# Kernel optimization log

Measured on AMD Instinct MI355X. Metric: run time of the kernel, lower is better.

Reference implementation:

```python
import jax, jax.numpy as jnp
import numpy as np

B, T, D = 4, 2048, 256
KQ, V, H = 16, 16, 8
SCALE = float(np.sqrt(KQ))


def _lin(key, din, dout):
    k1, k2 = jax.random.split(key)
    lim = 1.0 / np.sqrt(din)
    w = jax.random.uniform(k1, (din, dout), minval=-lim, maxval=lim, dtype=jnp.float32)
    b = jax.random.uniform(k2, (dout,), minval=-lim, maxval=lim, dtype=jnp.float32)
    return w, b


def setup_inputs() -> dict:
    key = jax.random.key(0)
    ks = jax.random.split(key, 14)
    x = jax.random.normal(ks[0], (B, 3, T), dtype=jnp.float32)
    h = jax.random.normal(ks[1], (B, D, T), dtype=jnp.float32)
    q_w1, q_b1 = _lin(ks[2], D, KQ * H)
    q_w2, q_b2 = _lin(ks[3], KQ * H, KQ * H)
    k_w1, k_b1 = _lin(ks[4], D, KQ * H)
    k_w2, k_b2 = _lin(ks[5], KQ * H, KQ * H)
    v_w1, v_b1 = _lin(ks[6], D, V * H)
    v_w2, v_b2 = _lin(ks[7], V * H, V * H)
    xm_w1, xm_b1 = _lin(ks[8], V * H, V * H)
    xm_w2, xm_b2 = _lin(ks[9], V * H, H)
    ho_w, ho_b = _lin(ks[10], V * H, D)
    # GVP: Wh [v_in, dim_h], Wu [dim_h, v_out]; torch init = randn
    gvp_Wh = jax.random.normal(ks[11], (H, H), dtype=jnp.float32)
    gvp_Wu = jax.random.normal(ks[12], (H, 1), dtype=jnp.float32)
    return dict(x=x, h=h,
                q_w1=q_w1, q_b1=q_b1, q_w2=q_w2, q_b2=q_b2,
                k_w1=k_w1, k_b1=k_b1, k_w2=k_w2, k_b2=k_b2,
                v_w1=v_w1, v_b1=v_b1, v_w2=v_w2, v_b2=v_b2,
                xm_w1=xm_w1, xm_b1=xm_b1, xm_w2=xm_w2, xm_b2=xm_b2,
                ho_w=ho_w, ho_b=ho_b, gvp_Wh=gvp_Wh, gvp_Wu=gvp_Wu)


def _mlp(x, w1, b1, w2, b2):
    return jax.nn.silu(x @ w1 + b1) @ w2 + b2


def _rotate_half(t):
    # interleaved pairs (x1,x2) -> (-x2, x1), lucidrains rotary convention
    t2 = t.reshape(t.shape[:-1] + (t.shape[-1] // 2, 2))
    a, b = t2[..., 0], t2[..., 1]
    return jnp.stack((-b, a), axis=-1).reshape(t.shape)


def _rope(t):
    # t: [B, H, T, KQ]
    seq = t.shape[-2]
    inv = 1.0 / (10000.0 ** (jnp.arange(0, KQ, 2, dtype=jnp.float32) / KQ))
    f = jnp.arange(seq, dtype=jnp.float32)[:, None] * inv[None, :]   # [T, KQ/2]
    f = jnp.repeat(f, 2, axis=-1)                                    # [T, KQ]
    return t * jnp.cos(f) + _rotate_half(t) * jnp.sin(f)


def _forward(x, h,
             q_w1, q_b1, q_w2, q_b2,
             k_w1, k_b1, k_w2, k_b2,
             v_w1, v_b1, v_w2, v_b2,
             xm_w1, xm_b1, xm_w2, xm_b2,
             ho_w, ho_b, gvp_Wh, gvp_Wu):
    b, _, t = x.shape
    h_m = jnp.transpose(h, (0, 2, 1)).reshape(b * t, D)     # merge_time_dim
    q = _mlp(h_m, q_w1, q_b1, q_w2, q_b2)                   # [B*T, KQ*H]
    k = _mlp(h_m, k_w1, k_b1, k_w2, k_b2)
    v = _mlp(h_m, v_w1, v_b1, v_w2, v_b2)                   # [B*T, V*H]
    v_x = _mlp(v, xm_w1, xm_b1, xm_w2, xm_b2)               # [B*T, H]

    q = q.reshape(b, t, H, KQ).transpose(0, 2, 1, 3)        # [B,H,T,KQ]
    k = k.reshape(b, t, H, KQ).transpose(0, 2, 1, 3)
    v4 = v.reshape(b, t, H, V).transpose(0, 2, 1, 3)        # [B,H,T,V]
    v_x = v_x.reshape(b, t, H).transpose(0, 2, 1)           # [B,H,T]

    q = _rope(q)
    k = _rope(k)

    attn = jax.nn.softmax(
        jnp.einsum('bhtd,bhsd->bhts', q, k) / SCALE, axis=-1)  # [B,H,T,T]

    h_upd = jnp.einsum('bhts,bhsd->bhtd', attn, v4)         # [B,H,T,V]
    h_upd = h_upd.transpose(0, 2, 1, 3).reshape(b, t, H * V)
    h_upd = (h_upd @ ho_w + ho_b).transpose(0, 2, 1)        # [B,D,T]
    h_out = h + h_upd

    attn_w = attn * v_x[:, :, None, :]                      # weight key axis s
    gamma = attn_w.sum(axis=-1)                             # [B,H,T]
    weighted_x = jnp.einsum('bhij,bdj->bhdi', attn_w, x)    # [B,H,3,T]
    x_head = gamma[:, :, None, :] * x[:, None, :, :] - weighted_x  # [B,H,3,T]
    x_upd = x_head.transpose(0, 3, 1, 2).reshape(b * t, H, 3)      # [B*T,H,3]

    # GVP vector branch (scalar branch does not affect returned vectors)
    Vh = jnp.einsum('bvc,vh->bhc', x_upd, gvp_Wh)           # [B*T,H,3]
    Vu = jnp.einsum('bhc,hu->buc', Vh, gvp_Wu)              # [B*T,1,3]
    gate = jnp.linalg.norm(Vu, axis=-1, keepdims=True)      # [B*T,1,1]
    delta = jax.nn.sigmoid(gate) * Vu                       # [B*T,1,3]
    delta = delta[:, 0, :].reshape(b, t, 3).transpose(0, 2, 1)  # separate_time_dim -> [B,3,T]
    x_out = x + delta
    return x_out, h_out


def reference(x, h,
              q_w1, q_b1, q_w2, q_b2,
              k_w1, k_b1, k_w2, k_b2,
              v_w1, v_b1, v_w2, v_b2,
              xm_w1, xm_b1, xm_w2, xm_b2,
              ho_w, ho_b, gvp_Wh, gvp_Wu):
    return _forward(x, h,
                    q_w1, q_b1, q_w2, q_b2,
                    k_w1, k_b1, k_w2, k_b2,
                    v_w1, v_b1, v_w2, v_b2,
                    xm_w1, xm_b1, xm_w2, xm_b2,
                    ho_w, ho_b, gvp_Wh, gvp_Wu)
```

## Files before the change

### kernel.cpp

```cpp
#include <hip/hip_runtime.h>
#include <hip/hip_bf16.h>
#include <math.h>

typedef __attribute__((ext_vector_type(8))) short s16x8;
typedef __attribute__((ext_vector_type(4))) float f32x4;

__device__ __forceinline__ float silu(float a) {
    return a / (1.f + __expf(-a));
}
__device__ __forceinline__ unsigned short f2b(float f) {
    __hip_bfloat16 h = __float2bfloat16(f);
    return *reinterpret_cast<unsigned short*>(&h);
}

__global__ __launch_bounds__(256) void wprep(
    const float* __restrict__ qw1, const float* __restrict__ kw1,
    const float* __restrict__ vw1, const float* __restrict__ qw2,
    const float* __restrict__ kw2, const float* __restrict__ vw2,
    const float* __restrict__ xmw1, const float* __restrict__ xmw2,
    const float* __restrict__ how,
    unsigned short* __restrict__ w1T, unsigned short* __restrict__ w2T,
    unsigned short* __restrict__ xm1T, unsigned short* __restrict__ xm2T,
    unsigned short* __restrict__ howT)
{
    int idx = blockIdx.x * 256 + threadIdx.x;
    if (idx < 98304) {
        int m = idx >> 15, r = idx & 32767;
        int n = r >> 8, k = r & 255;
        const float* src = (m == 0) ? qw1 : (m == 1) ? kw1 : vw1;
        w1T[idx] = f2b(src[k * 128 + n]);
    } else if (idx < 147456) {
        int r0 = idx - 98304;
        int m = r0 >> 14, r = r0 & 16383;
        int n = r >> 7, k = r & 127;
        const float* src = (m == 0) ? qw2 : (m == 1) ? kw2 : vw2;
        w2T[r0] = f2b(src[k * 128 + n]);
    } else if (idx < 163840) {
        int r = idx - 147456;
        int n = r >> 7, k = r & 127;
        xm1T[r] = f2b(xmw1[k * 128 + n]);
    } else if (idx < 165888) {
        int r = idx - 163840;
        int n = r >> 7, k = r & 127;
        xm2T[r] = (n < 8) ? f2b(xmw2[k * 8 + n]) : (unsigned short)0;
    } else if (idx < 198656) {
        int r = idx - 165888;
        int n = r >> 7, k = r & 127;
        howT[r] = f2b(how[k * 256 + n]);
    }
}

__global__ __launch_bounds__(256) void qkv_mfma(
    const float* __restrict__ x, const float* __restrict__ h,
    const float* __restrict__ qb1, const float* __restrict__ qb2,
    const float* __restrict__ kb1, const float* __restrict__ kb2,
    const float* __restrict__ vb1, const float* __restrict__ vb2,
    const float* __restrict__ xmb1, const float* __restrict__ xmb2,
    const unsigned short* __restrict__ w1T, const unsigned short* __restrict__ w2T,
    const unsigned short* __restrict__ xm1T, const unsigned short* __restrict__ xm2T,
    unsigned short* __restrict__ q_bf, unsigned short* __restrict__ k_bf,
    unsigned short* __restrict__ vT_bf)
{
    const int blk = blockIdx.x;
    const int b   = blk >> 7;
    const int t0  = (blk & 127) << 4;
    const int tid = threadIdx.x;
    const int nq   = tid >> 6;
    const int lane = tid & 63;
    const int m_   = lane & 15;
    const int quad = lane >> 4;

    __shared__ __align__(16) unsigned short hA[16][264];
    __shared__ __align__(16) unsigned short hidQ[16][136];
    __shared__ __align__(16) unsigned short hidK[16][136];
    __shared__ __align__(16) unsigned short hidV[16][136];
    __shared__ __align__(16) unsigned short voutA[16][136];
    __shared__ float vxs[16][8];

    #pragma unroll
    for (int g = 0; g < 4; g++) {
        float4 hv = *(const float4*)(h + ((size_t)(b * 256 + tid)) * 2048
                                       + t0 + g * 4);
        hA[g * 4 + 0][tid] = f2b(hv.x);
        hA[g * 4 + 1][tid] = f2b(hv.y);
        hA[g * 4 + 2][tid] = f2b(hv.z);
        hA[g * 4 + 3][tid] = f2b(hv.w);
    }
    __syncthreads();

    const f32x4 zero = {0.f, 0.f, 0.f, 0.f};

    {
        f32x4 aQ[2] = {zero, zero}, aK[2] = {zero, zero}, aV[2] = {zero, zero};
        #pragma unroll
        for (int kc = 0; kc < 8; kc++) {
            s16x8 af = *(const s16x8*)&hA[m_][kc * 32 + quad * 8];
            #pragma unroll
            for (int nt = 0; nt < 2; nt++) {
                size_t woff = (size_t)(nq * 32 + nt * 16 + m_) * 256
                            + kc * 32 + quad * 8;
                aQ[nt] = __builtin_amdgcn_mfma_f32_16x16x32_bf16(
                    af, *(const s16x8*)(w1T + woff), aQ[nt], 0, 0, 0);
                aK[nt] = __builtin_amdgcn_mfma_f32_16x16x32_bf16(
                    af, *(const s16x8*)(w1T + 32768 + woff), aK[nt], 0, 0, 0);
                aV[nt] = __builtin_amdgcn_mfma_f32_16x16x32_bf16(
                    af, *(const s16x8*)(w1T + 65536 + woff), aV[nt], 0, 0, 0);
            }
        }
        #pragma unroll
        for (int nt = 0; nt < 2; nt++) {
            int col = nq * 32 + nt * 16 + m_;
            float bq = qb1[col], bk = kb1[col], bv = vb1[col];
            #pragma unroll
            for (int i = 0; i < 4; i++) {
                hidQ[quad * 4 + i][col] = f2b(silu(aQ[nt][i] + bq));
                hidK[quad * 4 + i][col] = f2b(silu(aK[nt][i] + bk));
                hidV[quad * 4 + i][col] = f2b(silu(aV[nt][i] + bv));
            }
        }
    }
    __syncthreads();

    auto gemm2 = [&](const unsigned short* w2m,
                     unsigned short (*hid)[136], f32x4 acc[2]) {
        #pragma unroll
        for (int kc = 0; kc < 4; kc++) {
            s16x8 af = *(const s16x8*)&hid[m_][kc * 32 + quad * 8];
            #pragma unroll
            for (int nt = 0; nt < 2; nt++) {
                const s16x8 bf = *(const s16x8*)(w2m
                    + (size_t)(nq * 32 + nt * 16 + m_) * 128 + kc * 32 + quad * 8);
                acc[nt] = __builtin_amdgcn_mfma_f32_16x16x32_bf16(
                    af, bf, acc[nt], 0, 0, 0);
            }
        }
    };
    auto rope_store = [&](f32x4 acc[2], const float* b2,
                          unsigned short* dst, float scale) {
        #pragma unroll
        for (int nt = 0; nt < 2; nt++) {
            int col  = nq * 32 + nt * 16 + m_;
            int head = col >> 4, dim = col & 15;
            float inv = exp2f(-(float)(dim >> 1) * 0.125f * 13.28771238f);
            float bia = b2[col];
            #pragma unroll
            for (int i = 0; i < 4; i++) {
                int t = t0 + quad * 4 + i;
                float a  = acc[nt][i] + bia;
                float pr = __shfl_xor(a, 1);
                float f  = (float)t * inv;
                float cs = cosf(f), sn = sinf(f);
                float o  = (dim & 1) ? (a * cs + pr * sn) : (a * cs - pr * sn);
                dst[((size_t)(b * 8 + head) * 2048 + t) * 16 + dim] =
                    f2b(o * scale);
            }
        }
    };

    {
        f32x4 aQ[2] = {zero, zero}, aK[2] = {zero, zero}, aV[2] = {zero, zero};
        gemm2(w2T,         hidQ, aQ);
        gemm2(w2T + 16384, hidK, aK);
        gemm2(w2T + 32768, hidV, aV);
        rope_store(aQ, qb2, q_bf, 0.25f);
        rope_store(aK, kb2, k_bf, 1.0f);
        #pragma unroll
        for (int nt = 0; nt < 2; nt++) {
            int col = nq * 32 + nt * 16 + m_;
            float bia = vb2[col];
            #pragma unroll
            for (int i = 0; i < 4; i++)
                voutA[quad * 4 + i][col] = f2b(aV[nt][i] + bia);
        }
    }
    __syncthreads();

    {
        int col = tid >> 1, tg = tid & 1;
        s16x8 pk;
        #pragma unroll
        for (int e = 0; e < 8; e++)
            pk[e] = (short)voutA[tg * 8 + e][col];
        *(s16x8*)(vT_bf + ((size_t)(b * 8 + (col >> 4)) * 32 + (col & 15)) * 2048
                        + t0 + tg * 8) = pk;
    }
    {
        f32x4 acc[2] = {zero, zero};
        #pragma unroll
        for (int kc = 0; kc < 4; kc++) {
            s16x8 af = *(const s16x8*)&voutA[m_][kc * 32 + quad * 8];
            #pragma unroll
            for (int nt = 0; nt < 2; nt++) {
                const s16x8 bf = *(const s16x8*)(xm1T
                    + (size_t)(nq * 32 + nt * 16 + m_) * 128 + kc * 32 + quad * 8);
                acc[nt] = __builtin_amdgcn_mfma_f32_16x16x32_bf16(
                    af, bf, acc[nt], 0, 0, 0);
            }
        }
        #pragma unroll
        for (int nt = 0; nt < 2; nt++) {
            int col = nq * 32 + nt * 16 + m_;
            float bia = xmb1[col];
            #pragma unroll
            for (int i = 0; i < 4; i++)
                hidQ[quad * 4 + i][col] = f2b(silu(acc[nt][i] + bia));
        }
    }
    __syncthreads();

    if (nq == 0) {
        f32x4 a2 = zero;
        #pragma unroll
        for (int kc = 0; kc < 4; kc++) {
            s16x8 af = *(const s16x8*)&hidQ[m_][kc * 32 + quad * 8];
            const s16x8 bf = *(const s16x8*)(xm2T
                + (size_t)m_ * 128 + kc * 32 + quad * 8);
            a2 = __builtin_amdgcn_mfma_f32_16x16x32_bf16(af, bf, a2, 0, 0, 0);
        }
        if (m_ < 8) {
            float bia = xmb2[m_];
            #pragma unroll
            for (int i = 0; i < 4; i++)
                vxs[quad * 4 + i][m_] = a2[i] + bia;
        }
    }
    __syncthreads();

    #pragma unroll
    for (int r = 0; r < 2; r++) {
        int i  = tid + r * 256;
        int hh = i >> 6, c = (i >> 4) & 3, tt = i & 15;
        float val = vxs[tt][hh];
        if (c)
            val *= x[((size_t)(b * 3 + (c - 1))) * 2048 + t0 + tt];
        vT_bf[((size_t)(b * 8 + hh) * 32 + 16 + c) * 2048 + t0 + tt] = f2b(val);
    }
    if (tid < 192) {
        int hh = tid / 24, rem = tid % 24;
        int c  = 20 + (rem >> 1), tg = rem & 1;
        s16x8 z = {0,0,0,0,0,0,0,0};
        *(s16x8*)(vT_bf + ((size_t)(b * 8 + hh) * 32 + c) * 2048
                        + t0 + tg * 8) = z;
    }
}

__global__ __launch_bounds__(64) void attn_mfma(
    const unsigned short* __restrict__ q_bf,
    const unsigned short* __restrict__ k_bf,
    const unsigned short* __restrict__ vT_bf,
    float* __restrict__ opart)
{
    const int blk  = blockIdx.x;
    const int sp   = blk >> 10;
    const int bh   = (blk >> 5) & 31;
    const int qs   = (blk & 31) << 6;
    const int lane = threadIdx.x;
    const int m_   = lane & 15;
    const int quad = lane >> 4;

    __shared__ __align__(16) unsigned short Elds[4][2][16 * 72];

    const s16x8 zs = {0, 0, 0, 0, 0, 0, 0, 0};
    const f32x4 zero = {0.f, 0.f, 0.f, 0.f};

    s16x8 qfrag[4];
    #pragma unroll
    for (int qt = 0; qt < 4; qt++) {
        qfrag[qt] = zs;
        if (quad < 2)
            qfrag[qt] = *(const s16x8*)(q_bf +
                ((size_t)(bh * 2048 + qs + qt * 16 + m_) * 16 + quad * 8));
    }

    f32x4 O0[4], O1[4];
    float lsq[4];
    #pragma unroll
    for (int qt = 0; qt < 4; qt++) {
        O0[qt] = zero; O1[qt] = zero; lsq[qt] = 0.f;
    }

    const unsigned short* kb = k_bf + ((size_t)bh * 2048 + sp * 1024) * 16;
    const unsigned short* vb = vT_bf + (size_t)bh * 32 * 2048 + sp * 1024;

    for (int kt = 0; kt < 16; kt++) {
        const int k0 = kt * 64;
        const int buf = kt & 1;

        s16x8 kf[4];
        #pragma unroll
        for (int n = 0; n < 4; n++) {
            kf[n] = zs;
            if (quad < 2)
                kf[n] = *(const s16x8*)(kb +
                      ((size_t)(k0 + n * 16 + m_) * 16 + quad * 8));
        }
        s16x8 vf0[2], vf1[2];
        #pragma unroll
        for (int c = 0; c < 2; c++) {
            vf0[c] = *(const s16x8*)(vb + (size_t)m_ * 2048
                                        + k0 + c * 32 + quad * 8);
            vf1[c] = *(const s16x8*)(vb + (size_t)(16 + m_) * 2048
                                        + k0 + c * 32 + quad * 8);
        }

        #pragma unroll
        for (int qt = 0; qt < 4; qt++) {
            #pragma unroll
            for (int n = 0; n < 4; n++) {
                f32x4 E = __builtin_amdgcn_mfma_f32_16x16x32_bf16(
                    kf[n], qfrag[qt], zero, 0, 0, 0);
                float e0 = __expf(E[0]);
                float e1 = __expf(E[1]);
                float e2 = __expf(E[2]);
                float e3 = __expf(E[3]);
                lsq[qt] += e0 + e1 + e2 + e3;
                uint2 pk;
                pk.x = (unsigned)f2b(e0) | ((unsigned)f2b(e1) << 16);
                pk.y = (unsigned)f2b(e2) | ((unsigned)f2b(e3) << 16);
                *(uint2*)&Elds[qt][buf][m_ * 72 + n * 16 + quad * 4] = pk;
            }
        }
        __builtin_amdgcn_s_waitcnt(0xc07f);

        #pragma unroll
        for (int qt = 0; qt < 4; qt++) {
            #pragma unroll
            for (int c = 0; c < 2; c++) {
                s16x8 af = *(const s16x8*)
                    &Elds[qt][buf][m_ * 72 + c * 32 + quad * 8];
                O0[qt] = __builtin_amdgcn_mfma_f32_16x16x32_bf16(
                    af, vf0[c], O0[qt], 0, 0, 0);
                O1[qt] = __builtin_amdgcn_mfma_f32_16x16x32_bf16(
                    af, vf1[c], O1[qt], 0, 0, 0);
            }
        }
    }

    #pragma unroll
    for (int qt = 0; qt < 4; qt++) {
        float s = lsq[qt];
        s += __shfl_xor(s, 16);
        s += __shfl_xor(s, 32);
        float* opb = opart + ((size_t)(sp * 32 + bh) * 2048 + qs + qt * 16) * 24;
        #pragma unroll
        for (int i = 0; i < 4; i++) {
            int row = quad * 4 + i;
            float* ob = opb + row * 24;
            ob[m_] = O0[qt][i];
            if (m_ < 4) ob[16 + m_] = O1[qt][i];
        }
        if (quad == 0) opb[m_ * 24 + 20] = s;
    }
}

__global__ __launch_bounds__(256) void epi_kernel(
    const float* __restrict__ opart, const unsigned short* __restrict__ howT,
    const float* __restrict__ x, const float* __restrict__ hin,
    const float* __restrict__ hob,
    const float* __restrict__ Wh, const float* __restrict__ Wu,
    float* __restrict__ out)
{
    const int blk = blockIdx.x;
    const int b  = blk >> 7;
    const int t0 = (blk & 127) << 4;
    const int tid = threadIdx.x;
    const int nq   = tid >> 6;
    const int lane = tid & 63;
    const int m_   = lane & 15;
    const int quad = lane >> 4;
    const size_t half = (size_t)32 * 2048 * 24;

    __shared__ __align__(16) unsigned short hvA[16][136];
    __shared__ float linv[8][16];
    __shared__ float gamma[8][16], wx[8][3][16];
    __shared__ float weff[8];

    if (tid < 128) {
        int hh = tid >> 4, tt = tid & 15;
        size_t off = ((size_t)(b * 8 + hh) * 2048 + t0 + tt) * 24 + 20;
        linv[hh][tt] = 1.f / (opart[off] + opart[half + off]);
    } else if (tid < 136) {
        int v = tid - 128;
        float s = 0.f;
        for (int j = 0; j < 8; j++) s += Wh[v * 8 + j] * Wu[j];
        weff[v] = s;
    }
    __syncthreads();

    #pragma unroll
    for (int r = 0; r < 8; r++) {
        int i = tid + r * 256;
        int jj = i >> 4, tt = i & 15;
        size_t off = ((size_t)(b * 8 + (jj >> 4)) * 2048 + t0 + tt) * 24
                   + (jj & 15);
        hvA[tt][jj] =
            f2b((opart[off] + opart[half + off]) * linv[jj >> 4][tt]);
    }
    #pragma unroll
    for (int r = 0; r < 2; r++) {
        int i = tid + r * 256;
        int hh = i >> 6, c = (i >> 4) & 3, tt = i & 15;
        size_t off = ((size_t)(b * 8 + hh) * 2048 + t0 + tt) * 24 + 16 + c;
        float v = (opart[off] + opart[half + off]) * linv[hh][tt];
        if (c == 0) gamma[hh][tt] = v; else wx[hh][c - 1][tt] = v;
    }
    __syncthreads();

    const f32x4 zero = {0.f, 0.f, 0.f, 0.f};
    #pragma unroll
    for (int nt = 0; nt < 4; nt++) {
        int col = nq * 64 + nt * 16 + m_;
        f32x4 acc = zero;
        #pragma unroll
        for (int kc = 0; kc < 4; kc++) {
            s16x8 af = *(const s16x8*)&hvA[m_][kc * 32 + quad * 8];
            const s16x8 bf = *(const s16x8*)(howT
                + (size_t)col * 128 + kc * 32 + quad * 8);
            acc = __builtin_amdgcn_mfma_f32_16x16x32_bf16(af, bf, acc, 0, 0, 0);
        }
        float bia = hob[col];
        size_t base = ((size_t)b * 256 + col) * 2048 + t0 + quad * 4;
        float4 hold = *(const float4*)(hin + base);
        float4 hres;
        hres.x = hold.x + acc[0] + bia;
        hres.y = hold.y + acc[1] + bia;
        hres.z = hold.z + acc[2] + bia;
        hres.w = hold.w + acc[3] + bia;
        *(float4*)(out + 24576 + base) = hres;
    }

    if (tid < 16) {
        int tt = tid;
        int t = t0 + tt;
        float Vu[3], xv[3];
        #pragma unroll
        for (int c = 0; c < 3; c++) {
            xv[c] = x[((size_t)b * 3 + c) * 2048 + t];
            float s = 0.f;
            #pragma unroll
            for (int v = 0; v < 8; v++)
                s += (gamma[v][tt] * xv[c] - wx[v][c][tt]) * weff[v];
            Vu[c] = s;
        }
        float gate = sqrtf(Vu[0]*Vu[0] + Vu[1]*Vu[1] + Vu[2]*Vu[2]);
        float sg = 1.f / (1.f + __expf(-gate));
        #pragma unroll
        for (int c = 0; c < 3; c++)
            out[((size_t)b * 3 + c) * 2048 + t] = xv[c] + sg * Vu[c];
    }
}

extern "C" void kernel_launch(void* const* d_in, const int* in_sizes, int n_in,
                              void* d_out, int out_size, void* d_ws,
                              size_t ws_size, hipStream_t stream)
{
    const float* x    = (const float*)d_in[0];
    const float* h    = (const float*)d_in[1];
    const float* qw1  = (const float*)d_in[2];
    const float* qb1  = (const float*)d_in[3];
    const float* qw2  = (const float*)d_in[4];
    const float* qb2  = (const float*)d_in[5];
    const float* kw1  = (const float*)d_in[6];
    const float* kb1  = (const float*)d_in[7];
    const float* kw2  = (const float*)d_in[8];
    const float* kb2  = (const float*)d_in[9];
    const float* vw1  = (const float*)d_in[10];
    const float* vb1  = (const float*)d_in[11];
    const float* vw2  = (const float*)d_in[12];
    const float* vb2  = (const float*)d_in[13];
    const float* xmw1 = (const float*)d_in[14];
    const float* xmb1 = (const float*)d_in[15];
    const float* xmw2 = (const float*)d_in[16];
    const float* xmb2 = (const float*)d_in[17];
    const float* how  = (const float*)d_in[18];
    const float* hob  = (const float*)d_in[19];
    const float* Wh   = (const float*)d_in[20];
    const float* Wu   = (const float*)d_in[21];
    float* out = (float*)d_out;

    unsigned short* q_bf  = (unsigned short*)d_ws;
    unsigned short* k_bf  = q_bf + (size_t)32 * 2048 * 16;
    unsigned short* vT_bf = k_bf + (size_t)32 * 2048 * 16;
    float* opart = (float*)(vT_bf + (size_t)32 * 32 * 2048);
    unsigned short* w1T  = (unsigned short*)(opart + (size_t)2 * 32 * 2048 * 24);
    unsigned short* w2T  = w1T + 98304;
    unsigned short* xm1T = w2T + 49152;
    unsigned short* xm2T = xm1T + 16384;
    unsigned short* howT = xm2T + 2048;

    wprep<<<776, 256, 0, stream>>>(qw1, kw1, vw1, qw2, kw2, vw2, xmw1, xmw2,
                                   how, w1T, w2T, xm1T, xm2T, howT);
    qkv_mfma<<<512, 256, 0, stream>>>(
        x, h, qb1, qb2, kb1, kb2, vb1, vb2, xmb1, xmb2,
        w1T, w2T, xm1T, xm2T, q_bf, k_bf, vT_bf);
    attn_mfma<<<2048, 64, 0, stream>>>(q_bf, k_bf, vT_bf, opart);
    epi_kernel<<<512, 256, 0, stream>>>(opart, howT, x, h, hob, Wh, Wu, out);
}
```

Baseline: 183.9 us.

## Split QKV projection into per-role blocks and attention keys into four splits

The QKV kernel now launches three times as many blocks, and each block computes only one of Q, K or V. Only V blocks continue into the xm MLP path. Attention splits the key range four ways instead of two, doubling the attention grid, and the epilogue sums four partial buffers. The aim is more parallelism and occupancy on a wide GPU. The cost is that every QKV block reloads the h tile three times and there is extra partial-sum traffic, which needs larger workspace.

```diff
diff --git a/kernel.cpp b/kernel.cpp
--- a/kernel.cpp
+++ b/kernel.cpp
@@ -61,19 +61,19 @@
     unsigned short* __restrict__ q_bf, unsigned short* __restrict__ k_bf,
     unsigned short* __restrict__ vT_bf)
 {
-    const int blk = blockIdx.x;
-    const int b   = blk >> 7;
-    const int t0  = (blk & 127) << 4;
-    const int tid = threadIdx.x;
+    const int blk  = blockIdx.x;
+    const int role = blk >> 9;
+    const int tb   = blk & 511;
+    const int b    = tb >> 7;
+    const int t0   = (tb & 127) << 4;
+    const int tid  = threadIdx.x;
     const int nq   = tid >> 6;
     const int lane = tid & 63;
     const int m_   = lane & 15;
     const int quad = lane >> 4;
 
     __shared__ __align__(16) unsigned short hA[16][264];
-    __shared__ __align__(16) unsigned short hidQ[16][136];
-    __shared__ __align__(16) unsigned short hidK[16][136];
-    __shared__ __align__(16) unsigned short hidV[16][136];
+    __shared__ __align__(16) unsigned short hidA[16][136];
     __shared__ __align__(16) unsigned short voutA[16][136];
     __shared__ float vxs[16][8];
 
@@ -89,54 +89,51 @@
     __syncthreads();
 
     const f32x4 zero = {0.f, 0.f, 0.f, 0.f};
+    const float* b1 = (role == 0) ? qb1 : (role == 1) ? kb1 : vb1;
+    const float* b2 = (role == 0) ? qb2 : (role == 1) ? kb2 : vb2;
+    const unsigned short* w1m = w1T + role * 32768;
+    const unsigned short* w2m = w2T + role * 16384;
 
     {
-        f32x4 aQ[2] = {zero, zero}, aK[2] = {zero, zero}, aV[2] = {zero, zero};
+        f32x4 acc[2] = {zero, zero};
         #pragma unroll
         for (int kc = 0; kc < 8; kc++) {
             s16x8 af = *(const s16x8*)&hA[m_][kc * 32 + quad * 8];
             #pragma unroll
             for (int nt = 0; nt < 2; nt++) {
-                size_t woff = (size_t)(nq * 32 + nt * 16 + m_) * 256
-                            + kc * 32 + quad * 8;
-                aQ[nt] = __builtin_amdgcn_mfma_f32_16x16x32_bf16(
-                    af, *(const s16x8*)(w1T + woff), aQ[nt], 0, 0, 0);
-                aK[nt] = __builtin_amdgcn_mfma_f32_16x16x32_bf16(
-                    af, *(const s16x8*)(w1T + 32768 + woff), aK[nt], 0, 0, 0);
-                aV[nt] = __builtin_amdgcn_mfma_f32_16x16x32_bf16(
-                    af, *(const s16x8*)(w1T + 65536 + woff), aV[nt], 0, 0, 0);
-            }
-        }
-        #pragma unroll
-        for (int nt = 0; nt < 2; nt++) {
-            int col = nq * 32 + nt * 16 + m_;
-            float bq = qb1[col], bk = kb1[col], bv = vb1[col];
-            #pragma unroll
-            for (int i = 0; i < 4; i++) {
-                hidQ[quad * 4 + i][col] = f2b(silu(aQ[nt][i] + bq));
-                hidK[quad * 4 + i][col] = f2b(silu(aK[nt][i] + bk));
-                hidV[quad * 4 + i][col] = f2b(silu(aV[nt][i] + bv));
-            }
-        }
-    }
-    __syncthreads();
-
-    auto gemm2 = [&](const unsigned short* w2m,
-                     unsigned short (*hid)[136], f32x4 acc[2]) {
-        #pragma unroll
-        for (int kc = 0; kc < 4; kc++) {
-            s16x8 af = *(const s16x8*)&hid[m_][kc * 32 + quad * 8];
-            #pragma unroll
-            for (int nt = 0; nt < 2; nt++) {
-                const s16x8 bf = *(const s16x8*)(w2m
-                    + (size_t)(nq * 32 + nt * 16 + m_) * 128 + kc * 32 + quad * 8);
+                const s16x8 bf = *(const s16x8*)(w1m
+                    + (size_t)(nq * 32 + nt * 16 + m_) * 256 + kc * 32 + quad * 8);
                 acc[nt] = __builtin_amdgcn_mfma_f32_16x16x32_bf16(
                     af, bf, acc[nt], 0, 0, 0);
             }
         }
-    };
-    auto rope_store = [&](f32x4 acc[2], const float* b2,
-                          unsigned short* dst, float scale) {
+        #pragma unroll
+        for (int nt = 0; nt < 2; nt++) {
+            int col = nq * 32 + nt * 16 + m_;
+            float bia = b1[col];
+            #pragma unroll
+            for (int i = 0; i < 4; i++)
+                hidA[quad * 4 + i][col] = f2b(silu(acc[nt][i] + bia));
+        }
+    }
+    __syncthreads();
+
+    f32x4 acc[2] = {zero, zero};
+    #pragma unroll
+    for (int kc = 0; kc < 4; kc++) {
+        s16x8 af = *(const s16x8*)&hidA[m_][kc * 32 + quad * 8];
+        #pragma unroll
+        for (int nt = 0; nt < 2; nt++) {
+            const s16x8 bf = *(const s16x8*)(w2m
+                + (size_t)(nq * 32 + nt * 16 + m_) * 128 + kc * 32 + quad * 8);
+            acc[nt] = __builtin_amdgcn_mfma_f32_16x16x32_bf16(
+                af, bf, acc[nt], 0, 0, 0);
+        }
+    }
+
+    if (role < 2) {
+        unsigned short* dst = (role == 0) ? q_bf : k_bf;
+        float scale = (role == 0) ? 0.25f : 1.0f;
         #pragma unroll
         for (int nt = 0; nt < 2; nt++) {
             int col  = nq * 32 + nt * 16 + m_;
@@ -155,23 +152,16 @@
                     f2b(o * scale);
             }
         }
-    };
-
-    {
-        f32x4 aQ[2] = {zero, zero}, aK[2] = {zero, zero}, aV[2] = {zero, zero};
-        gemm2(w2T,         hidQ, aQ);
-        gemm2(w2T + 16384, hidK, aK);
-        gemm2(w2T + 32768, hidV, aV);
-        rope_store(aQ, qb2, q_bf, 0.25f);
-        rope_store(aK, kb2, k_bf, 1.0f);
-        #pragma unroll
-        for (int nt = 0; nt < 2; nt++) {
-            int col = nq * 32 + nt * 16 + m_;
-            float bia = vb2[col];
-            #pragma unroll
-            for (int i = 0; i < 4; i++)
-                voutA[quad * 4 + i][col] = f2b(aV[nt][i] + bia);
-        }
+        return;
+    }
+
+    #pragma unroll
+    for (int nt = 0; nt < 2; nt++) {
+        int col = nq * 32 + nt * 16 + m_;
+        float bia = b2[col];
+        #pragma unroll
+        for (int i = 0; i < 4; i++)
+            voutA[quad * 4 + i][col] = f2b(acc[nt][i] + bia);
     }
     __syncthreads();
 
@@ -185,7 +175,7 @@
                         + t0 + tg * 8) = pk;
     }
     {
-        f32x4 acc[2] = {zero, zero};
+        f32x4 a1[2] = {zero, zero};
         #pragma unroll
         for (int kc = 0; kc < 4; kc++) {
             s16x8 af = *(const s16x8*)&voutA[m_][kc * 32 + quad * 8];
@@ -193,17 +183,18 @@
             for (int nt = 0; nt < 2; nt++) {
                 const s16x8 bf = *(const s16x8*)(xm1T
                     + (size_t)(nq * 32 + nt * 16 + m_) * 128 + kc * 32 + quad * 8);
-                acc[nt] = __builtin_amdgcn_mfma_f32_16x16x32_bf16(
-                    af, bf, acc[nt], 0, 0, 0);
+                a1[nt] = __builtin_amdgcn_mfma_f32_16x16x32_bf16(
+                    af, bf, a1[nt], 0, 0, 0);
             }
         }
+        __syncthreads();
         #pragma unroll
         for (int nt = 0; nt < 2; nt++) {
             int col = nq * 32 + nt * 16 + m_;
             float bia = xmb1[col];
             #pragma unroll
             for (int i = 0; i < 4; i++)
-                hidQ[quad * 4 + i][col] = f2b(silu(acc[nt][i] + bia));
+                hidA[quad * 4 + i][col] = f2b(silu(a1[nt][i] + bia));
         }
     }
     __syncthreads();
@@ -212,7 +203,7 @@
         f32x4 a2 = zero;
         #pragma unroll
         for (int kc = 0; kc < 4; kc++) {
-            s16x8 af = *(const s16x8*)&hidQ[m_][kc * 32 + quad * 8];
+            s16x8 af = *(const s16x8*)&hidA[m_][kc * 32 + quad * 8];
             const s16x8 bf = *(const s16x8*)(xm2T
                 + (size_t)m_ * 128 + kc * 32 + quad * 8);
             a2 = __builtin_amdgcn_mfma_f32_16x16x32_bf16(af, bf, a2, 0, 0, 0);
@@ -279,10 +270,10 @@
         O0[qt] = zero; O1[qt] = zero; lsq[qt] = 0.f;
     }
 
-    const unsigned short* kb = k_bf + ((size_t)bh * 2048 + sp * 1024) * 16;
-    const unsigned short* vb = vT_bf + (size_t)bh * 32 * 2048 + sp * 1024;
-
-    for (int kt = 0; kt < 16; kt++) {
+    const unsigned short* kb = k_bf + ((size_t)bh * 2048 + sp * 512) * 16;
+    const unsigned short* vb = vT_bf + (size_t)bh * 32 * 2048 + sp * 512;
+
+    for (int kt = 0; kt < 8; kt++) {
         const int k0 = kt * 64;
         const int buf = kt & 1;
 
@@ -368,17 +359,22 @@
     const int lane = tid & 63;
     const int m_   = lane & 15;
     const int quad = lane >> 4;
-    const size_t half = (size_t)32 * 2048 * 24;
+    const size_t qtr = (size_t)32 * 2048 * 24;
 
     __shared__ __align__(16) unsigned short hvA[16][136];
     __shared__ float linv[8][16];
     __shared__ float gamma[8][16], wx[8][3][16];
     __shared__ float weff[8];
 
+    auto comb = [&](size_t off) -> float {
+        return opart[off] + opart[qtr + off] + opart[2 * qtr + off]
+             + opart[3 * qtr + off];
+    };
+
     if (tid < 128) {
         int hh = tid >> 4, tt = tid & 15;
         size_t off = ((size_t)(b * 8 + hh) * 2048 + t0 + tt) * 24 + 20;
-        linv[hh][tt] = 1.f / (opart[off] + opart[half + off]);
+        linv[hh][tt] = 1.f / comb(off);
     } else if (tid < 136) {
         int v = tid - 128;
         float s = 0.f;
@@ -393,15 +389,14 @@
         int jj = i >> 4, tt = i & 15;
         size_t off = ((size_t)(b * 8 + (jj >> 4)) * 2048 + t0 + tt) * 24
                    + (jj & 15);
-        hvA[tt][jj] =
-            f2b((opart[off] + opart[half + off]) * linv[jj >> 4][tt]);
+        hvA[tt][jj] = f2b(comb(off) * linv[jj >> 4][tt]);
     }
     #pragma unroll
     for (int r = 0; r < 2; r++) {
         int i = tid + r * 256;
         int hh = i >> 6, c = (i >> 4) & 3, tt = i & 15;
         size_t off = ((size_t)(b * 8 + hh) * 2048 + t0 + tt) * 24 + 16 + c;
-        float v = (opart[off] + opart[half + off]) * linv[hh][tt];
+        float v = comb(off) * linv[hh][tt];
         if (c == 0) gamma[hh][tt] = v; else wx[hh][c - 1][tt] = v;
     }
     __syncthreads();
@@ -482,7 +477,7 @@
     unsigned short* k_bf  = q_bf + (size_t)32 * 2048 * 16;
     unsigned short* vT_bf = k_bf + (size_t)32 * 2048 * 16;
     float* opart = (float*)(vT_bf + (size_t)32 * 32 * 2048);
-    unsigned short* w1T  = (unsigned short*)(opart + (size_t)2 * 32 * 2048 * 24);
+    unsigned short* w1T  = (unsigned short*)(opart + (size_t)4 * 32 * 2048 * 24);
     unsigned short* w2T  = w1T + 98304;
     unsigned short* xm1T = w2T + 49152;
     unsigned short* xm2T = xm1T + 16384;
@@ -490,9 +485,9 @@
 
     wprep<<<776, 256, 0, stream>>>(qw1, kw1, vw1, qw2, kw2, vw2, xmw1, xmw2,
                                    how, w1T, w2T, xm1T, xm2T, howT);
-    qkv_mfma<<<512, 256, 0, stream>>>(
+    qkv_mfma<<<1536, 256, 0, stream>>>(
         x, h, qb1, qb2, kb1, kb2, vb1, vb2, xmb1, xmb2,
         w1T, w2T, xm1T, xm2T, q_bf, k_bf, vT_bf);
-    attn_mfma<<<2048, 64, 0, stream>>>(q_bf, k_bf, vT_bf, opart);
+    attn_mfma<<<4096, 64, 0, stream>>>(q_bf, k_bf, vT_bf, opart);
     epi_kernel<<<512, 256, 0, stream>>>(opart, howT, x, h, hob, Wh, Wu, out);
 }
```

After: 188.2 us. +2.3%, slower.
